# Optimization experiments

Measured on AMD Instinct MI355X. Metric: run time of the kernel, lower is better.

Reference implementation:

```python
import jax, jax.numpy as jnp
import numpy as np


def setup_inputs() -> dict:
    key = jax.random.key(0)
    k1, k2, k3 = jax.random.split(key, 3)
    n, seq_len, hidden = 100000, 4, 128
    n_edges = 1600000
    semantics = jax.random.normal(k1, (n, seq_len, hidden), dtype=jnp.float32)
    attention_masks = jnp.ones((n, seq_len, hidden), dtype=jnp.float32)
    W = jax.random.normal(k2, (hidden, hidden), dtype=jnp.float32) * (1.0 / np.sqrt(hidden))
    edge_index = jax.random.randint(k3, (n_edges, 2), 0, n, dtype=jnp.int64)
    return {"semantics": semantics, "attention_masks": attention_masks, "W": W, "edge_index": edge_index}


def reference(semantics, attention_masks, W, edge_index):
    # semantics: (n, seq_len, hidden); only token 0 is used.
    # edge_index: (E, 2) = adj.nonzero(); col 0 = source (gather), col 1 = target (scatter).
    n = semantics.shape[0]
    h = semantics[:, 0] @ W                         # (n, hidden)
    src = h[edge_index[:, 0]]                       # (E, hidden) gather
    tgt = edge_index[:, 1]
    sums = jax.ops.segment_sum(src, tgt, num_segments=n)            # (n, hidden)
    cnt = jax.ops.segment_sum(jnp.ones((edge_index.shape[0],), dtype=h.dtype), tgt, num_segments=n)
    h_mean = sums / jnp.maximum(cnt, 1.0)[:, None]  # scatter_mean; untouched rows stay 0
    return jax.nn.gelu(h_mean, approximate=False)
```

## Files before the change

kernel.cpp:

```cpp
#include <hip/hip_runtime.h>
#include <math.h>


#define SLOT 64

__global__ void fill_csr(const int* __restrict__ edges, int* __restrict__ cnt,
                         int* __restrict__ csr, int n_edges) {
    int e = blockIdx.x * blockDim.x + threadIdx.x;
    if (e < n_edges) {
        int2 p = ((const int2*)edges)[e];
        int pos = atomicAdd(&cnt[p.y], 1);
        if (pos < SLOT) csr[(size_t)p.y * SLOT + pos] = p.x;
    }
}

__global__ __launch_bounds__(256) void gather_mean(
        const float* __restrict__ sem, const int* __restrict__ cnt,
        const int* __restrict__ csr, float* __restrict__ mean, int n) {
    int gid  = blockIdx.x * blockDim.x + threadIdx.x;
    int node = gid >> 6;
    int lane = gid & 63;
    if (node >= n) return;

    int deg = cnt[node];
    int m   = min(deg, SLOT);
    int sv  = (lane < m) ? csr[(size_t)node * SLOT + lane] : 0;

    const int half = lane >> 5;
    const int q    = lane & 31;

    float4 acc = make_float4(0.f, 0.f, 0.f, 0.f);

    int j = 0;
    for (; j + 8 <= m; j += 8) {
        int s0 = __shfl(sv, j + 0 + half);
        int s1 = __shfl(sv, j + 2 + half);
        int s2 = __shfl(sv, j + 4 + half);
        int s3 = __shfl(sv, j + 6 + half);
        float4 v0 = ((const float4*)(sem + (size_t)s0 * 512))[q];
        float4 v1 = ((const float4*)(sem + (size_t)s1 * 512))[q];
        float4 v2 = ((const float4*)(sem + (size_t)s2 * 512))[q];
        float4 v3 = ((const float4*)(sem + (size_t)s3 * 512))[q];
        acc.x += v0.x; acc.y += v0.y; acc.z += v0.z; acc.w += v0.w;
        acc.x += v1.x; acc.y += v1.y; acc.z += v1.z; acc.w += v1.w;
        acc.x += v2.x; acc.y += v2.y; acc.z += v2.z; acc.w += v2.w;
        acc.x += v3.x; acc.y += v3.y; acc.z += v3.z; acc.w += v3.w;
    }
    for (; j + 2 <= m; j += 2) {
        int s = __shfl(sv, j + half);
        float4 v = ((const float4*)(sem + (size_t)s * 512))[q];
        acc.x += v.x; acc.y += v.y; acc.z += v.z; acc.w += v.w;
    }
    if (j < m) {
        int s = __shfl(sv, j);
        if (half == 0) {
            float4 v = ((const float4*)(sem + (size_t)s * 512))[q];
            acc.x += v.x; acc.y += v.y; acc.z += v.z; acc.w += v.w;
        }
    }

    float4 oth;
    oth.x = __shfl(acc.x, (lane + 32) & 63);
    oth.y = __shfl(acc.y, (lane + 32) & 63);
    oth.z = __shfl(acc.z, (lane + 32) & 63);
    oth.w = __shfl(acc.w, (lane + 32) & 63);

    if (half == 0) {
        float inv = 1.0f / fmaxf((float)deg, 1.0f);
        float4 t = make_float4((acc.x + oth.x) * inv, (acc.y + oth.y) * inv,
                               (acc.z + oth.z) * inv, (acc.w + oth.w) * inv);
        ((float4*)(mean + (size_t)node * 128))[q] = t;
    }
}

__device__ __forceinline__ float gelu_exact(float x) {
    return 0.5f * x * (1.0f + erff(x * 0.70710678118654752f));
}
__device__ __forceinline__ void fma4(float m, const float4 w, float4& a) {
    a.x = fmaf(m, w.x, a.x); a.y = fmaf(m, w.y, a.y);
    a.z = fmaf(m, w.z, a.z); a.w = fmaf(m, w.w, a.w);
}

__global__ __launch_bounds__(256, 2) void finalize_kernel(
        const float* __restrict__ W, float* __restrict__ io, int n) {
    __shared__ float Wl[128 * 128];
    __shared__ float ml[32 * 128];

    for (int i = threadIdx.x; i < 128 * 32; i += 256)
        ((float4*)Wl)[i] = ((const float4*)W)[i];

    const int r  = threadIdx.x >> 5;
    const int cg = threadIdx.x & 31;
    const int rowsPerIter = 32 * gridDim.x;

    for (int row0 = blockIdx.x * 32; row0 < n; row0 += rowsPerIter) {
        __syncthreads();
        #pragma unroll
        for (int p = 0; p < 4; p++) {
            int fid = threadIdx.x + 256 * p;
            int rr = fid >> 5, k4 = fid & 31;
            int row = row0 + rr;
            if (row < n)
                ((float4*)ml)[fid] = ((const float4*)(io + (size_t)row * 128))[k4];
        }
        __syncthreads();

        float4 a0, a1, a2, a3;
        a0 = a1 = a2 = a3 = make_float4(0.f, 0.f, 0.f, 0.f);
        const float4* m0 = (const float4*)(ml + (r     ) * 128);
        const float4* m1 = (const float4*)(ml + (r +  8) * 128);
        const float4* m2 = (const float4*)(ml + (r + 16) * 128);
        const float4* m3 = (const float4*)(ml + (r + 24) * 128);

        #pragma unroll 2
        for (int k4 = 0; k4 < 32; k4++) {
            float4 mv0 = m0[k4], mv1 = m1[k4], mv2 = m2[k4], mv3 = m3[k4];
            const float* p0 = (const float*)&mv0;
            const float* p1 = (const float*)&mv1;
            const float* p2 = (const float*)&mv2;
            const float* p3 = (const float*)&mv3;
            #pragma unroll
            for (int kk = 0; kk < 4; kk++) {
                float4 wv = ((const float4*)(Wl + (k4 * 4 + kk) * 128))[cg];
                fma4(p0[kk], wv, a0);
                fma4(p1[kk], wv, a1);
                fma4(p2[kk], wv, a2);
                fma4(p3[kk], wv, a3);
            }
        }

        int rowA = row0 + r;
        if (rowA < n) {
            float4 g = make_float4(gelu_exact(a0.x), gelu_exact(a0.y),
                                   gelu_exact(a0.z), gelu_exact(a0.w));
            ((float4*)(io + (size_t)rowA * 128))[cg] = g;
        }
        int rowB = row0 + r + 8;
        if (rowB < n) {
            float4 g = make_float4(gelu_exact(a1.x), gelu_exact(a1.y),
                                   gelu_exact(a1.z), gelu_exact(a1.w));
            ((float4*)(io + (size_t)rowB * 128))[cg] = g;
        }
        int rowC = row0 + r + 16;
        if (rowC < n) {
            float4 g = make_float4(gelu_exact(a2.x), gelu_exact(a2.y),
                                   gelu_exact(a2.z), gelu_exact(a2.w));
            ((float4*)(io + (size_t)rowC * 128))[cg] = g;
        }
        int rowD = row0 + r + 24;
        if (rowD < n) {
            float4 g = make_float4(gelu_exact(a3.x), gelu_exact(a3.y),
                                   gelu_exact(a3.z), gelu_exact(a3.w));
            ((float4*)(io + (size_t)rowD * 128))[cg] = g;
        }
    }
}

extern "C" void kernel_launch(void* const* d_in, const int* in_sizes, int n_in,
                              void* d_out, int out_size, void* d_ws, size_t ws_size,
                              hipStream_t stream) {
    const float* sem   = (const float*)d_in[0];
    const float* W     = (const float*)d_in[2];
    const int*   edges = (const int*)d_in[3];

    const int n       = in_sizes[0] / (4 * 128);
    const int n_edges = in_sizes[3] / 2;

    char* p = (char*)d_ws;
    int* cnt = (int*)p;   p += (((size_t)n * 4) + 15) & ~(size_t)15;
    int* csr = (int*)p;

    hipMemsetAsync(cnt, 0, (size_t)n * 4, stream);

    const int T = 256;
    fill_csr   <<<(n_edges + T - 1) / T, T, 0, stream>>>(edges, cnt, csr, n_edges);

    const int gblocks = (int)(((long long)n * 64 + T - 1) / T);
    gather_mean<<<gblocks, T, 0, stream>>>(sem, cnt, csr, (float*)d_out, n);

    finalize_kernel<<<512, T, 0, stream>>>(W, (float*)d_out, n);
}
```

Baseline: 581.9 us.

## Batch edges per thread, deepen gather unroll, restructure finalize GEMM tiling

fill_csr now handles four edges per thread using vector int4 loads, so there are fewer threads and more atomics in flight per thread. gather_mean unrolls its gather loop to 16 neighbours per iteration with 8 outstanding float4 loads, raising memory-level parallelism. finalize_kernel drops the shared-memory copy of W and reads W rows straight from global/L2 into registers. Each block now computes 64 rows with 8 rows per thread across 1024 blocks, which lowers LDS use but adds register pressure and repeated global reads of W.

```diff
diff --git a/kernel.cpp b/kernel.cpp
--- a/kernel.cpp
+++ b/kernel.cpp
@@ -4,13 +4,27 @@
 
 #define SLOT 64
 
-__global__ void fill_csr(const int* __restrict__ edges, int* __restrict__ cnt,
-                         int* __restrict__ csr, int n_edges) {
-    int e = blockIdx.x * blockDim.x + threadIdx.x;
-    if (e < n_edges) {
-        int2 p = ((const int2*)edges)[e];
-        int pos = atomicAdd(&cnt[p.y], 1);
-        if (pos < SLOT) csr[(size_t)p.y * SLOT + pos] = p.x;
+__global__ __launch_bounds__(256) void fill_csr(const int* __restrict__ edges,
+        int* __restrict__ cnt, int* __restrict__ csr, int n_edges) {
+    int t = blockIdx.x * blockDim.x + threadIdx.x;
+    int base = t * 4;
+    if (base + 3 < n_edges) {
+        int4 a = ((const int4*)edges)[t * 2];
+        int4 b = ((const int4*)edges)[t * 2 + 1];
+        int src[4] = {a.x, a.z, b.x, b.z};
+        int tgt[4] = {a.y, a.w, b.y, b.w};
+        int pos[4];
+        #pragma unroll
+        for (int i = 0; i < 4; i++) pos[i] = atomicAdd(&cnt[tgt[i]], 1);
+        #pragma unroll
+        for (int i = 0; i < 4; i++)
+            if (pos[i] < SLOT) csr[(size_t)tgt[i] * SLOT + pos[i]] = src[i];
+    } else if (base < n_edges) {
+        for (int e = base; e < n_edges; e++) {
+            int2 p = ((const int2*)edges)[e];
+            int pos = atomicAdd(&cnt[p.y], 1);
+            if (pos < SLOT) csr[(size_t)p.y * SLOT + pos] = p.x;
+        }
     }
 }
 
@@ -32,19 +46,18 @@
     float4 acc = make_float4(0.f, 0.f, 0.f, 0.f);
 
     int j = 0;
-    for (; j + 8 <= m; j += 8) {
-        int s0 = __shfl(sv, j + 0 + half);
-        int s1 = __shfl(sv, j + 2 + half);
-        int s2 = __shfl(sv, j + 4 + half);
-        int s3 = __shfl(sv, j + 6 + half);
-        float4 v0 = ((const float4*)(sem + (size_t)s0 * 512))[q];
-        float4 v1 = ((const float4*)(sem + (size_t)s1 * 512))[q];
-        float4 v2 = ((const float4*)(sem + (size_t)s2 * 512))[q];
-        float4 v3 = ((const float4*)(sem + (size_t)s3 * 512))[q];
-        acc.x += v0.x; acc.y += v0.y; acc.z += v0.z; acc.w += v0.w;
-        acc.x += v1.x; acc.y += v1.y; acc.z += v1.z; acc.w += v1.w;
-        acc.x += v2.x; acc.y += v2.y; acc.z += v2.z; acc.w += v2.w;
-        acc.x += v3.x; acc.y += v3.y; acc.z += v3.z; acc.w += v3.w;
+    for (; j + 16 <= m; j += 16) {
+        int s[8];
+        #pragma unroll
+        for (int u = 0; u < 8; u++) s[u] = __shfl(sv, j + 2 * u + half);
+        float4 v[8];
+        #pragma unroll
+        for (int u = 0; u < 8; u++)
+            v[u] = ((const float4*)(sem + (size_t)s[u] * 512))[q];
+        #pragma unroll
+        for (int u = 0; u < 8; u++) {
+            acc.x += v[u].x; acc.y += v[u].y; acc.z += v[u].z; acc.w += v[u].w;
+        }
     }
     for (; j + 2 <= m; j += 2) {
         int s = __shfl(sv, j + half);
@@ -81,22 +94,18 @@
     a.z = fmaf(m, w.z, a.z); a.w = fmaf(m, w.w, a.w);
 }
 
-__global__ __launch_bounds__(256, 2) void finalize_kernel(
+__global__ __launch_bounds__(256) void finalize_kernel(
         const float* __restrict__ W, float* __restrict__ io, int n) {
-    __shared__ float Wl[128 * 128];
-    __shared__ float ml[32 * 128];
+    __shared__ float ml[64 * 128];
 
-    for (int i = threadIdx.x; i < 128 * 32; i += 256)
-        ((float4*)Wl)[i] = ((const float4*)W)[i];
+    const int cg = threadIdx.x & 31;
+    const int rb = threadIdx.x >> 5;
+    const int rowsPerIter = 64 * gridDim.x;
 
-    const int r  = threadIdx.x >> 5;
-    const int cg = threadIdx.x & 31;
-    const int rowsPerIter = 32 * gridDim.x;
-
-    for (int row0 = blockIdx.x * 32; row0 < n; row0 += rowsPerIter) {
+    for (int row0 = blockIdx.x * 64; row0 < n; row0 += rowsPerIter) {
         __syncthreads();
         #pragma unroll
-        for (int p = 0; p < 4; p++) {
+        for (int p = 0; p < 8; p++) {
             int fid = threadIdx.x + 256 * p;
             int rr = fid >> 5, k4 = fid & 31;
             int row = row0 + rr;
@@ -105,53 +114,40 @@
         }
         __syncthreads();
 
-        float4 a0, a1, a2, a3;
-        a0 = a1 = a2 = a3 = make_float4(0.f, 0.f, 0.f, 0.f);
-        const float4* m0 = (const float4*)(ml + (r     ) * 128);
-        const float4* m1 = (const float4*)(ml + (r +  8) * 128);
-        const float4* m2 = (const float4*)(ml + (r + 16) * 128);
-        const float4* m3 = (const float4*)(ml + (r + 24) * 128);
+        float4 acc[8];
+        #pragma unroll
+        for (int i = 0; i < 8; i++) acc[i] = make_float4(0.f, 0.f, 0.f, 0.f);
 
-        #pragma unroll 2
-        for (int k4 = 0; k4 < 32; k4++) {
-            float4 mv0 = m0[k4], mv1 = m1[k4], mv2 = m2[k4], mv3 = m3[k4];
-            const float* p0 = (const float*)&mv0;
-            const float* p1 = (const float*)&mv1;
-            const float* p2 = (const float*)&mv2;
-            const float* p3 = (const float*)&mv3;
+        const float* mbase = ml + rb * 8 * 128;
+
+        for (int kc = 0; kc < 16; kc++) {
+            float4 wreg[8];
             #pragma unroll
-            for (int kk = 0; kk < 4; kk++) {
-                float4 wv = ((const float4*)(Wl + (k4 * 4 + kk) * 128))[cg];
-                fma4(p0[kk], wv, a0);
-                fma4(p1[kk], wv, a1);
-                fma4(p2[kk], wv, a2);
-                fma4(p3[kk], wv, a3);
+            for (int u = 0; u < 8; u++)
+                wreg[u] = ((const float4*)(W + (size_t)(kc * 8 + u) * 128))[cg];
+            #pragma unroll
+            for (int rr = 0; rr < 8; rr++) {
+                const float4* mrow = (const float4*)(mbase + rr * 128);
+                float4 mlo = mrow[kc * 2], mhi = mrow[kc * 2 + 1];
+                fma4(mlo.x, wreg[0], acc[rr]);
+                fma4(mlo.y, wreg[1], acc[rr]);
+                fma4(mlo.z, wreg[2], acc[rr]);
+                fma4(mlo.w, wreg[3], acc[rr]);
+                fma4(mhi.x, wreg[4], acc[rr]);
+                fma4(mhi.y, wreg[5], acc[rr]);
+                fma4(mhi.z, wreg[6], acc[rr]);
+                fma4(mhi.w, wreg[7], acc[rr]);
             }
         }
 
-        int rowA = row0 + r;
-        if (rowA < n) {
-            float4 g = make_float4(gelu_exact(a0.x), gelu_exact(a0.y),
-                                   gelu_exact(a0.z), gelu_exact(a0.w));
-            ((float4*)(io + (size_t)rowA * 128))[cg] = g;
-        }
-        int rowB = row0 + r + 8;
-        if (rowB < n) {
-            float4 g = make_float4(gelu_exact(a1.x), gelu_exact(a1.y),
-                                   gelu_exact(a1.z), gelu_exact(a1.w));
-            ((float4*)(io + (size_t)rowB * 128))[cg] = g;
-        }
-        int rowC = row0 + r + 16;
-        if (rowC < n) {
-            float4 g = make_float4(gelu_exact(a2.x), gelu_exact(a2.y),
-                                   gelu_exact(a2.z), gelu_exact(a2.w));
-            ((float4*)(io + (size_t)rowC * 128))[cg] = g;
-        }
-        int rowD = row0 + r + 24;
-        if (rowD < n) {
-            float4 g = make_float4(gelu_exact(a3.x), gelu_exact(a3.y),
-                                   gelu_exact(a3.z), gelu_exact(a3.w));
-            ((float4*)(io + (size_t)rowD * 128))[cg] = g;
+        #pragma unroll
+        for (int rr = 0; rr < 8; rr++) {
+            int row = row0 + rb * 8 + rr;
+            if (row < n) {
+                float4 g = make_float4(gelu_exact(acc[rr].x), gelu_exact(acc[rr].y),
+                                       gelu_exact(acc[rr].z), gelu_exact(acc[rr].w));
+                ((float4*)(io + (size_t)row * 128))[cg] = g;
+            }
         }
     }
 }
@@ -173,10 +169,11 @@
     hipMemsetAsync(cnt, 0, (size_t)n * 4, stream);
 
     const int T = 256;
-    fill_csr   <<<(n_edges + T - 1) / T, T, 0, stream>>>(edges, cnt, csr, n_edges);
+    const int fthreads = (n_edges + 3) / 4;
+    fill_csr   <<<(fthreads + T - 1) / T, T, 0, stream>>>(edges, cnt, csr, n_edges);
 
     const int gblocks = (int)(((long long)n * 64 + T - 1) / T);
     gather_mean<<<gblocks, T, 0, stream>>>(sem, cnt, csr, (float*)d_out, n);
 
-    finalize_kernel<<<512, T, 0, stream>>>(W, (float*)d_out, n);
+    finalize_kernel<<<1024, T, 0, stream>>>(W, (float*)d_out, n);
 }
```

New measurement: 623.8 us. +7.2%, slower.
